# Optimization experiments

Hardware: AMD Instinct MI355X
Metric: run time of the kernel (lower is better)

## Reference

```python
import jax, jax.numpy as jnp
import numpy as np

B, CQ, CV, H, W, D = 1, 8, 64, 64, 64, 64


def setup_inputs() -> dict:
    key = jax.random.key(0)
    kq, kk, kv = jax.random.split(key, 3)
    return {
        "proj_query": jax.random.normal(kq, (B, CQ, H, W, D), dtype=jnp.float32),
        "proj_key": jax.random.normal(kk, (B, CQ, H, W, D), dtype=jnp.float32),
        "proj_value": jax.random.normal(kv, (B, CV, H, W, D), dtype=jnp.float32),
    }


def reference(proj_query, proj_key, proj_value):
    b, c, h, w, d = proj_query.shape
    # Axis-wise affinities, all laid out as [b, w, h, d, axis_len] to match the
    # torch concat/softmax layout. x/y/z index the attended H/W/D positions.
    energy_H = jnp.einsum('bchwd,bcxwd->bwhdx', proj_query, proj_key)  # [b,w,h,d,H]
    energy_W = jnp.einsum('bchwd,bchyd->bwhdy', proj_query, proj_key)  # [b,w,h,d,W]
    energy_D = jnp.einsum('bchwd,bchwz->bwhdz', proj_query, proj_key)  # [b,w,h,d,D]

    # Diagonal -inf masks on the H and D axes (the W axis is left unmasked,
    # exactly as in the original module -- it keeps the self position once).
    mask_H = jnp.where(jnp.eye(h, dtype=bool), -jnp.inf, 0.0).astype(energy_H.dtype)
    mask_D = jnp.where(jnp.eye(d, dtype=bool), -jnp.inf, 0.0).astype(energy_D.dtype)
    energy_H = energy_H + mask_H[None, None, :, None, :]   # mask where h == x
    energy_D = energy_D + mask_D[None, None, None, :, :]   # mask where d == z

    # Joint softmax over the concatenated H+W+D axis.
    attn = jax.nn.softmax(jnp.concatenate([energy_H, energy_W, energy_D], axis=-1), axis=-1)
    att_H = attn[..., :h]            # [b,w,h,d,H]
    att_W = attn[..., h:h + w]       # [b,w,h,d,W]
    att_D = attn[..., h + w:]        # [b,w,h,d,D]

    out_H = jnp.einsum('bcxwd,bwhdx->bchwd', proj_value, att_H)
    out_W = jnp.einsum('bchyd,bwhdy->bchwd', proj_value, att_W)
    out_D = jnp.einsum('bchwz,bwhdz->bchwd', proj_value, att_D)
    return out_H + out_W + out_D
```

## Files before the change

kernel.cpp:

```cpp
#include <hip/hip_runtime.h>
#include <math.h>

#define SQC 262144
#define SH  4096
#define SW  64

template <int AXIS>
__global__ __launch_bounds__(1024) void k_stats_hw(
    const float* __restrict__ Q, const float* __restrict__ K,
    float* __restrict__ m_out, float* __restrict__ l_out)
{
    __shared__ float Kc[8][8][64];

    const int tid   = threadIdx.x;
    const int d     = tid & 63;
    const int g     = tid >> 6;
    const int fixed = blockIdx.x & 63;
    const int mbase = (blockIdx.x >> 6) << 4;

    const int MS = (AXIS == 0) ? SH : SW;
    const int FS = (AXIS == 0) ? SW : SH;

    const int qoff = (AXIS == 0) ? ((mbase + g) * SH + fixed * SW + d)
                                 : (fixed * SH + (mbase + g) * SW + d);
    float q[8];
#pragma unroll
    for (int c = 0; c < 8; ++c) q[c] = Q[c * SQC + qoff];

    float m = -INFINITY, l = 0.f;

#pragma unroll 1
    for (int kc = 0; kc < 8; ++kc) {
#pragma unroll
        for (int j = 0; j < 4; ++j) {
            const int t  = tid + j * 1024;
            const int xi = t >> 9;
            const int c  = (t >> 6) & 7;
            const int dd = t & 63;
            Kc[xi][c][dd] = K[c * SQC + (kc * 8 + xi) * MS + fixed * FS + dd];
        }
        __syncthreads();

        float e[8];
#pragma unroll
        for (int xi = 0; xi < 8; ++xi) {
            float a = 0.f;
#pragma unroll
            for (int c = 0; c < 8; ++c)
                a = fmaf(q[c], Kc[xi][c][d], a);
            if (AXIS == 0 && (kc * 8 + xi) == (mbase + g)) a = -INFINITY;
            e[xi] = a;
        }
        float cm = e[0];
#pragma unroll
        for (int xi = 1; xi < 8; ++xi) cm = fmaxf(cm, e[xi]);
        const float nm = fmaxf(m, cm);
        float s = 0.f;
#pragma unroll
        for (int xi = 0; xi < 8; ++xi) s += __expf(e[xi] - nm);
        l = fmaf(l, __expf(m - nm), s);
        m = nm;
        __syncthreads();
    }

    m_out[qoff] = m;
    l_out[qoff] = l;
}

__global__ __launch_bounds__(256) void k_dpass(
    const float* __restrict__ Q, const float* __restrict__ K, const float* __restrict__ V,
    const float* __restrict__ mH, const float* __restrict__ lH,
    const float* __restrict__ mW, const float* __restrict__ lW,
    float* __restrict__ M_out, float* __restrict__ RL_out,
    float* __restrict__ out)
{
    __shared__ float KD[8][64];
    __shared__ float VDT[64][68];
    __shared__ float AZ[64][64];
    __shared__ float sm[4][64], sl[4][64], Ms[64], RLs[64];

    const int tid = threadIdx.x;
    const int d   = tid & 63;
    const int zq  = tid >> 6;
    const int h = blockIdx.x >> 6, w = blockIdx.x & 63;
    const int base = h * SH + w * SW;

    if (tid < 128) {
        const int c = tid >> 4, dv = (tid & 15) * 4;
        *reinterpret_cast<float4*>(&KD[c][dv]) =
            *reinterpret_cast<const float4*>(&K[c * SQC + base + dv]);
    }
#pragma unroll
    for (int j = 0; j < 4; ++j) {
        const int c0 = 16 * zq + 4 * j;
        float4 v;
        v.x = V[(c0 + 0) * SQC + base + d];
        v.y = V[(c0 + 1) * SQC + base + d];
        v.z = V[(c0 + 2) * SQC + base + d];
        v.w = V[(c0 + 3) * SQC + base + d];
        *reinterpret_cast<float4*>(&VDT[d][c0]) = v;
    }

    float q[8];
#pragma unroll
    for (int c = 0; c < 8; ++c) q[c] = Q[c * SQC + base + d];
    __syncthreads();

    float e[16];
#pragma unroll
    for (int zi = 0; zi < 16; ++zi) {
        const int z = zq * 16 + zi;
        float a = 0.f;
#pragma unroll
        for (int c = 0; c < 8; ++c)
            a = fmaf(q[c], KD[c][z], a);
        e[zi] = (z == d) ? -INFINITY : a;
    }
    float pm = e[0];
#pragma unroll
    for (int zi = 1; zi < 16; ++zi) pm = fmaxf(pm, e[zi]);
    float pl = 0.f;
#pragma unroll
    for (int zi = 0; zi < 16; ++zi) pl += __expf(e[zi] - pm);
    sm[zq][d] = pm;
    sl[zq][d] = pl;
    __syncthreads();

    if (tid < 64) {
        const float m0 = sm[0][d], m1 = sm[1][d], m2 = sm[2][d], m3 = sm[3][d];
        const float mD = fmaxf(fmaxf(m0, m1), fmaxf(m2, m3));
        const float lD = sl[0][d] * __expf(m0 - mD) + sl[1][d] * __expf(m1 - mD)
                       + sl[2][d] * __expf(m2 - mD) + sl[3][d] * __expf(m3 - mD);
        const int idx = base + d;
        const float mh = mH[idx], mw = mW[idx];
        const float M  = fmaxf(fmaxf(mh, mw), mD);
        const float L  = lH[idx] * __expf(mh - M) + lW[idx] * __expf(mw - M)
                       + lD * __expf(mD - M);
        const float RL = 1.0f / L;
        M_out[idx]  = M;
        RL_out[idx] = RL;
        Ms[d]  = M;
        RLs[d] = RL;
    }
    __syncthreads();

    {
        const float M = Ms[d], RL = RLs[d];
#pragma unroll
        for (int zi = 0; zi < 16; ++zi) {
            const int z = zq * 16 + zi;
            AZ[z][d] = (z == d) ? 0.f : __expf(e[zi] - M) * RL;
        }
    }
    __syncthreads();

    const int ci = tid >> 4, dj = tid & 15;
    float acc[4][4];
#pragma unroll
    for (int a = 0; a < 4; ++a)
#pragma unroll
        for (int b = 0; b < 4; ++b) acc[a][b] = 0.f;

#pragma unroll 8
    for (int z = 0; z < 64; ++z) {
        const float4 va = *reinterpret_cast<const float4*>(&VDT[z][4 * ci]);
        const float4 vb = *reinterpret_cast<const float4*>(&AZ[z][4 * dj]);
        const float av[4] = {va.x, va.y, va.z, va.w};
        const float bv[4] = {vb.x, vb.y, vb.z, vb.w};
#pragma unroll
        for (int a = 0; a < 4; ++a)
#pragma unroll
            for (int b = 0; b < 4; ++b)
                acc[a][b] = fmaf(av[a], bv[b], acc[a][b]);
    }

#pragma unroll
    for (int a = 0; a < 4; ++a) {
        const float4 o = make_float4(acc[a][0], acc[a][1], acc[a][2], acc[a][3]);
        *reinterpret_cast<float4*>(&out[(4 * ci + a) * SQC + base + 4 * dj]) = o;
    }
}

__global__ __launch_bounds__(1024) void k_hpass(
    const float* __restrict__ Q, const float* __restrict__ K, const float* __restrict__ V,
    const float* __restrict__ m_ws, const float* __restrict__ rl_ws,
    float* __restrict__ out)
{
    __shared__ float Kx[4][8][64];
    __shared__ float Vx[4][64][64];
    __shared__ float Ax[4][16][64];

    const int tid = threadIdx.x;
    const int d   = tid & 63;
    const int g   = tid >> 6;
    const int w     = blockIdx.x & 63;
    const int hbase = (blockIdx.x >> 6) << 4;

    const int h_e = hbase + g;
    float q[8];
#pragma unroll
    for (int c = 0; c < 8; ++c) q[c] = Q[c * SQC + h_e * SH + w * SW + d];
    const int qidx = h_e * SH + w * SW + d;
    const float m = m_ws[qidx], rl = rl_ws[qidx];

    const int co = g & 7, hh = g >> 3;
    float acc[8][8];
#pragma unroll
    for (int a = 0; a < 8; ++a)
#pragma unroll
        for (int b = 0; b < 8; ++b) acc[a][b] = 0.f;

#pragma unroll 1
    for (int xs = 0; xs < 16; ++xs) {
        const int x0 = xs * 4;
#pragma unroll
        for (int j = 0; j < 4; ++j) {
            const int u  = j * 1024 + tid;
            const int xi = u >> 10;
            const int c  = (u >> 4) & 63;
            const int dv = (u & 15) * 4;
            *reinterpret_cast<float4*>(&Vx[xi][c][dv]) =
                *reinterpret_cast<const float4*>(&V[c * SQC + (x0 + xi) * SH + w * SW + dv]);
        }
        if (tid < 512) {
            const int xi = tid >> 7;
            const int c  = (tid >> 4) & 7;
            const int dv = (tid & 15) * 4;
            *reinterpret_cast<float4*>(&Kx[xi][c][dv]) =
                *reinterpret_cast<const float4*>(&K[c * SQC + (x0 + xi) * SH + w * SW + dv]);
        }
        __syncthreads();

#pragma unroll
        for (int xi = 0; xi < 4; ++xi) {
            float e = 0.f;
#pragma unroll
            for (int c = 0; c < 8; ++c) e = fmaf(q[c], Kx[xi][c][d], e);
            Ax[xi][g][d] = ((x0 + xi) == h_e) ? 0.f : __expf(e - m) * rl;
        }
        __syncthreads();

#pragma unroll
        for (int xi = 0; xi < 4; ++xi) {
            float va[8], pa[8];
#pragma unroll
            for (int cc = 0; cc < 8; ++cc) va[cc] = Vx[xi][8 * co + cc][d];
#pragma unroll
            for (int aa = 0; aa < 8; ++aa) pa[aa] = Ax[xi][8 * hh + aa][d];
#pragma unroll
            for (int cc = 0; cc < 8; ++cc)
#pragma unroll
                for (int aa = 0; aa < 8; ++aa)
                    acc[cc][aa] = fmaf(va[cc], pa[aa], acc[cc][aa]);
        }
        __syncthreads();
    }

#pragma unroll
    for (int cc = 0; cc < 8; ++cc)
#pragma unroll
        for (int aa = 0; aa < 8; ++aa) {
            float* op = &out[(8 * co + cc) * SQC + (hbase + 8 * hh + aa) * SH + w * SW + d];
            *op += acc[cc][aa];
        }
}

__global__ __launch_bounds__(1024) void k_wpass(
    const float* __restrict__ Q, const float* __restrict__ K, const float* __restrict__ V,
    const float* __restrict__ m_ws, const float* __restrict__ rl_ws,
    float* __restrict__ out)
{
    __shared__ float Ky[4][8][64];
    __shared__ float Vy[4][64][64];
    __shared__ float Ay[4][16][64];

    const int tid = threadIdx.x;
    const int d   = tid & 63;
    const int g   = tid >> 6;
    const int h     = blockIdx.x & 63;
    const int wbase = (blockIdx.x >> 6) << 4;

    const int w_e = wbase + g;
    float q[8];
#pragma unroll
    for (int c = 0; c < 8; ++c) q[c] = Q[c * SQC + h * SH + w_e * SW + d];
    const int qidx = h * SH + w_e * SW + d;
    const float m = m_ws[qidx], rl = rl_ws[qidx];

    const int co = g & 7, wh = g >> 3;
    float acc[8][8];
#pragma unroll
    for (int a = 0; a < 8; ++a)
#pragma unroll
        for (int b = 0; b < 8; ++b) acc[a][b] = 0.f;

#pragma unroll 1
    for (int ys = 0; ys < 16; ++ys) {
        const int y0 = ys * 4;
#pragma unroll
        for (int j = 0; j < 4; ++j) {
            const int u  = j * 1024 + tid;
            const int yi = u >> 10;
            const int c  = (u >> 4) & 63;
            const int dv = (u & 15) * 4;
            *reinterpret_cast<float4*>(&Vy[yi][c][dv]) =
                *reinterpret_cast<const float4*>(&V[c * SQC + h * SH + (y0 + yi) * SW + dv]);
        }
        if (tid < 512) {
            const int yi = tid >> 7;
            const int c  = (tid >> 4) & 7;
            const int dv = (tid & 15) * 4;
            *reinterpret_cast<float4*>(&Ky[yi][c][dv]) =
                *reinterpret_cast<const float4*>(&K[c * SQC + h * SH + (y0 + yi) * SW + dv]);
        }
        __syncthreads();

#pragma unroll
        for (int yi = 0; yi < 4; ++yi) {
            float e = 0.f;
#pragma unroll
            for (int c = 0; c < 8; ++c) e = fmaf(q[c], Ky[yi][c][d], e);
            Ay[yi][g][d] = __expf(e - m) * rl;
        }
        __syncthreads();

#pragma unroll
        for (int yi = 0; yi < 4; ++yi) {
            float va[8], pa[8];
#pragma unroll
            for (int cc = 0; cc < 8; ++cc) va[cc] = Vy[yi][8 * co + cc][d];
#pragma unroll
            for (int ww = 0; ww < 8; ++ww) pa[ww] = Ay[yi][8 * wh + ww][d];
#pragma unroll
            for (int cc = 0; cc < 8; ++cc)
#pragma unroll
                for (int ww = 0; ww < 8; ++ww)
                    acc[cc][ww] = fmaf(va[cc], pa[ww], acc[cc][ww]);
        }
        __syncthreads();
    }

#pragma unroll
    for (int cc = 0; cc < 8; ++cc)
#pragma unroll
        for (int ww = 0; ww < 8; ++ww) {
            float* op = &out[(8 * co + cc) * SQC + h * SH + (wbase + 8 * wh + ww) * SW + d];
            *op += acc[cc][ww];
        }
}

extern "C" void kernel_launch(void* const* d_in, const int* in_sizes, int n_in,
                              void* d_out, int out_size, void* d_ws, size_t ws_size,
                              hipStream_t stream)
{
    const float* Q = (const float*)d_in[0];
    const float* K = (const float*)d_in[1];
    const float* V = (const float*)d_in[2];
    float* out = (float*)d_out;

    float* mH = (float*)d_ws;
    float* lH = mH + SQC;
    float* mW = lH + SQC;
    float* lW = mW + SQC;
    float* M  = lW + SQC;
    float* RL = M  + SQC;

    hipLaunchKernelGGL((k_stats_hw<0>), dim3(256), dim3(1024), 0, stream, Q, K, mH, lH);
    hipLaunchKernelGGL((k_stats_hw<1>), dim3(256), dim3(1024), 0, stream, Q, K, mW, lW);
    hipLaunchKernelGGL(k_dpass, dim3(4096), dim3(256), 0, stream, Q, K, V, mH, lH, mW, lW, M, RL, out);
    hipLaunchKernelGGL(k_hpass, dim3(256),  dim3(1024), 0, stream, Q, K, V, M, RL, out);
    hipLaunchKernelGGL(k_wpass, dim3(256),  dim3(1024), 0, stream, Q, K, V, M, RL, out);
}
```

Measured before the change: 352.2 us.

## Split H/W pass kernels across channel halves to double grid and cut shared memory

```diff
diff --git a/kernel.cpp b/kernel.cpp
--- a/kernel.cpp
+++ b/kernel.cpp
@@ -181,20 +181,21 @@
     }
 }
 
-__global__ __launch_bounds__(1024) void k_hpass(
+__global__ __launch_bounds__(1024, 8) void k_hpass(
     const float* __restrict__ Q, const float* __restrict__ K, const float* __restrict__ V,
     const float* __restrict__ m_ws, const float* __restrict__ rl_ws,
     float* __restrict__ out)
 {
-    __shared__ float Kx[4][8][64];
-    __shared__ float Vx[4][64][64];
-    __shared__ float Ax[4][16][64];
+    __shared__ float Kx[2][8][64];
+    __shared__ float Vx[2][32][64];
+    __shared__ float Ax[2][16][64];
 
     const int tid = threadIdx.x;
     const int d   = tid & 63;
     const int g   = tid >> 6;
     const int w     = blockIdx.x & 63;
-    const int hbase = (blockIdx.x >> 6) << 4;
+    const int hbase = ((blockIdx.x >> 6) & 3) << 4;
+    const int c0    = (blockIdx.x >> 8) << 5;
 
     const int h_e = hbase + g;
     float q[8];
@@ -203,36 +204,34 @@
     const int qidx = h_e * SH + w * SW + d;
     const float m = m_ws[qidx], rl = rl_ws[qidx];
 
-    const int co = g & 7, hh = g >> 3;
-    float acc[8][8];
+    const int co = g & 3, hg = g >> 2;
+    float acc[8][4];
 #pragma unroll
     for (int a = 0; a < 8; ++a)
 #pragma unroll
-        for (int b = 0; b < 8; ++b) acc[a][b] = 0.f;
+        for (int b = 0; b < 4; ++b) acc[a][b] = 0.f;
+
+    const int sv_xi = tid >> 9;
+    const int sv_c  = (tid >> 4) & 31;
+    const int sv_dv = (tid & 15) * 4;
+    const int sk_xi = tid >> 7;
+    const int sk_c  = (tid >> 4) & 7;
 
 #pragma unroll 1
-    for (int xs = 0; xs < 16; ++xs) {
-        const int x0 = xs * 4;
-#pragma unroll
-        for (int j = 0; j < 4; ++j) {
-            const int u  = j * 1024 + tid;
-            const int xi = u >> 10;
-            const int c  = (u >> 4) & 63;
-            const int dv = (u & 15) * 4;
-            *reinterpret_cast<float4*>(&Vx[xi][c][dv]) =
-                *reinterpret_cast<const float4*>(&V[c * SQC + (x0 + xi) * SH + w * SW + dv]);
-        }
-        if (tid < 512) {
-            const int xi = tid >> 7;
-            const int c  = (tid >> 4) & 7;
-            const int dv = (tid & 15) * 4;
-            *reinterpret_cast<float4*>(&Kx[xi][c][dv]) =
-                *reinterpret_cast<const float4*>(&K[c * SQC + (x0 + xi) * SH + w * SW + dv]);
-        }
-        __syncthreads();
-
-#pragma unroll
-        for (int xi = 0; xi < 4; ++xi) {
+    for (int ss = 0; ss < 32; ++ss) {
+        const int x0 = ss * 2;
+        *reinterpret_cast<float4*>(&Vx[sv_xi][sv_c][sv_dv]) =
+            *reinterpret_cast<const float4*>(
+                &V[(c0 + sv_c) * SQC + (x0 + sv_xi) * SH + w * SW + sv_dv]);
+        if (tid < 256) {
+            *reinterpret_cast<float4*>(&Kx[sk_xi][sk_c][sv_dv]) =
+                *reinterpret_cast<const float4*>(
+                    &K[sk_c * SQC + (x0 + sk_xi) * SH + w * SW + sv_dv]);
+        }
+        __syncthreads();
+
+#pragma unroll
+        for (int xi = 0; xi < 2; ++xi) {
             float e = 0.f;
 #pragma unroll
             for (int c = 0; c < 8; ++c) e = fmaf(q[c], Kx[xi][c][d], e);
@@ -241,16 +240,16 @@
         __syncthreads();
 
 #pragma unroll
-        for (int xi = 0; xi < 4; ++xi) {
-            float va[8], pa[8];
+        for (int xi = 0; xi < 2; ++xi) {
+            float va[8], pa[4];
 #pragma unroll
             for (int cc = 0; cc < 8; ++cc) va[cc] = Vx[xi][8 * co + cc][d];
 #pragma unroll
-            for (int aa = 0; aa < 8; ++aa) pa[aa] = Ax[xi][8 * hh + aa][d];
+            for (int aa = 0; aa < 4; ++aa) pa[aa] = Ax[xi][4 * hg + aa][d];
 #pragma unroll
             for (int cc = 0; cc < 8; ++cc)
 #pragma unroll
-                for (int aa = 0; aa < 8; ++aa)
+                for (int aa = 0; aa < 4; ++aa)
                     acc[cc][aa] = fmaf(va[cc], pa[aa], acc[cc][aa]);
         }
         __syncthreads();
@@ -259,26 +258,27 @@
 #pragma unroll
     for (int cc = 0; cc < 8; ++cc)
 #pragma unroll
-        for (int aa = 0; aa < 8; ++aa) {
-            float* op = &out[(8 * co + cc) * SQC + (hbase + 8 * hh + aa) * SH + w * SW + d];
+        for (int aa = 0; aa < 4; ++aa) {
+            float* op = &out[(c0 + 8 * co + cc) * SQC + (hbase + 4 * hg + aa) * SH + w * SW + d];
             *op += acc[cc][aa];
         }
 }
 
-__global__ __launch_bounds__(1024) void k_wpass(
+__global__ __launch_bounds__(1024, 8) void k_wpass(
     const float* __restrict__ Q, const float* __restrict__ K, const float* __restrict__ V,
     const float* __restrict__ m_ws, const float* __restrict__ rl_ws,
     float* __restrict__ out)
 {
-    __shared__ float Ky[4][8][64];
-    __shared__ float Vy[4][64][64];
-    __shared__ float Ay[4][16][64];
+    __shared__ float Ky[2][8][64];
+    __shared__ float Vy[2][32][64];
+    __shared__ float Ay[2][16][64];
 
     const int tid = threadIdx.x;
     const int d   = tid & 63;
     const int g   = tid >> 6;
     const int h     = blockIdx.x & 63;
-    const int wbase = (blockIdx.x >> 6) << 4;
+    const int wbase = ((blockIdx.x >> 6) & 3) << 4;
+    const int c0    = (blockIdx.x >> 8) << 5;
 
     const int w_e = wbase + g;
     float q[8];
@@ -287,36 +287,34 @@
     const int qidx = h * SH + w_e * SW + d;
     const float m = m_ws[qidx], rl = rl_ws[qidx];
 
-    const int co = g & 7, wh = g >> 3;
-    float acc[8][8];
+    const int co = g & 3, wg = g >> 2;
+    float acc[8][4];
 #pragma unroll
     for (int a = 0; a < 8; ++a)
 #pragma unroll
-        for (int b = 0; b < 8; ++b) acc[a][b] = 0.f;
+        for (int b = 0; b < 4; ++b) acc[a][b] = 0.f;
+
+    const int sv_yi = tid >> 9;
+    const int sv_c  = (tid >> 4) & 31;
+    const int sv_dv = (tid & 15) * 4;
+    const int sk_yi = tid >> 7;
+    const int sk_c  = (tid >> 4) & 7;
 
 #pragma unroll 1
-    for (int ys = 0; ys < 16; ++ys) {
-        const int y0 = ys * 4;
-#pragma unroll
-        for (int j = 0; j < 4; ++j) {
-            const int u  = j * 1024 + tid;
-            const int yi = u >> 10;
-            const int c  = (u >> 4) & 63;
-            const int dv = (u & 15) * 4;
-            *reinterpret_cast<float4*>(&Vy[yi][c][dv]) =
-                *reinterpret_cast<const float4*>(&V[c * SQC + h * SH + (y0 + yi) * SW + dv]);
-        }
-        if (tid < 512) {
-            const int yi = tid >> 7;
-            const int c  = (tid >> 4) & 7;
-            const int dv = (tid & 15) * 4;
-            *reinterpret_cast<float4*>(&Ky[yi][c][dv]) =
-                *reinterpret_cast<const float4*>(&K[c * SQC + h * SH + (y0 + yi) * SW + dv]);
-        }
-        __syncthreads();
-
-#pragma unroll
-        for (int yi = 0; yi < 4; ++yi) {
+    for (int ss = 0; ss < 32; ++ss) {
+        const int y0 = ss * 2;
+        *reinterpret_cast<float4*>(&Vy[sv_yi][sv_c][sv_dv]) =
+            *reinterpret_cast<const float4*>(
+                &V[(c0 + sv_c) * SQC + h * SH + (y0 + sv_yi) * SW + sv_dv]);
+        if (tid < 256) {
+            *reinterpret_cast<float4*>(&Ky[sk_yi][sk_c][sv_dv]) =
+                *reinterpret_cast<const float4*>(
+                    &K[sk_c * SQC + h * SH + (y0 + sk_yi) * SW + sv_dv]);
+        }
+        __syncthreads();
+
+#pragma unroll
+        for (int yi = 0; yi < 2; ++yi) {
             float e = 0.f;
 #pragma unroll
             for (int c = 0; c < 8; ++c) e = fmaf(q[c], Ky[yi][c][d], e);
@@ -325,17 +323,17 @@
         __syncthreads();
 
 #pragma unroll
-        for (int yi = 0; yi < 4; ++yi) {
-            float va[8], pa[8];
+        for (int yi = 0; yi < 2; ++yi) {
+            float va[8], pa[4];
 #pragma unroll
             for (int cc = 0; cc < 8; ++cc) va[cc] = Vy[yi][8 * co + cc][d];
 #pragma unroll
-            for (int ww = 0; ww < 8; ++ww) pa[ww] = Ay[yi][8 * wh + ww][d];
+            for (int aa = 0; aa < 4; ++aa) pa[aa] = Ay[yi][4 * wg + aa][d];
 #pragma unroll
             for (int cc = 0; cc < 8; ++cc)
 #pragma unroll
-                for (int ww = 0; ww < 8; ++ww)
-                    acc[cc][ww] = fmaf(va[cc], pa[ww], acc[cc][ww]);
+                for (int aa = 0; aa < 4; ++aa)
+                    acc[cc][aa] = fmaf(va[cc], pa[aa], acc[cc][aa]);
         }
         __syncthreads();
     }
@@ -343,9 +341,9 @@
 #pragma unroll
     for (int cc = 0; cc < 8; ++cc)
 #pragma unroll
-        for (int ww = 0; ww < 8; ++ww) {
-            float* op = &out[(8 * co + cc) * SQC + h * SH + (wbase + 8 * wh + ww) * SW + d];
-            *op += acc[cc][ww];
+        for (int aa = 0; aa < 4; ++aa) {
+            float* op = &out[(c0 + 8 * co + cc) * SQC + h * SH + (wbase + 4 * wg + aa) * SW + d];
+            *op += acc[cc][aa];
         }
 }
 
@@ -368,6 +366,6 @@
     hipLaunchKernelGGL((k_stats_hw<0>), dim3(256), dim3(1024), 0, stream, Q, K, mH, lH);
     hipLaunchKernelGGL((k_stats_hw<1>), dim3(256), dim3(1024), 0, stream, Q, K, mW, lW);
     hipLaunchKernelGGL(k_dpass, dim3(4096), dim3(256), 0, stream, Q, K, V, mH, lH, mW, lW, M, RL, out);
-    hipLaunchKernelGGL(k_hpass, dim3(256),  dim3(1024), 0, stream, Q, K, V, M, RL, out);
-    hipLaunchKernelGGL(k_wpass, dim3(256),  dim3(1024), 0, stream, Q, K, V, M, RL, out);
-}
+    hipLaunchKernelGGL(k_hpass, dim3(512),  dim3(1024), 0, stream, Q, K, V, M, RL, out);
+    hipLaunchKernelGGL(k_wpass, dim3(512),  dim3(1024), 0, stream, Q, K, V, M, RL, out);
+}
```

New measurement: 324.7 us. 1.08x faster.
